# Kernel optimization log

Hardware: AMD Instinct MI355X
Metric: run time of the kernel (lower is better)

The kernel has to match this reference:

```python
import jax, jax.numpy as jnp
import numpy as np

B, N, H, W = 1, 256, 32, 32
C_LIDAR, C_RGB, K, S = 64, 64, 16, 3
MLP3 = [128, 64, 64]


def _l2norm(x, eps=1e-12):
    n = jnp.linalg.norm(x, axis=-1, keepdims=True)
    return x / jnp.maximum(n, eps)


def _cal_sim(src, dst):
    # src [B,N,C], dst [B,M,C] -> [B,N,M,2] (cosine sim normalized two ways)
    s = _l2norm(src)
    d = _l2norm(dst)
    sim = jnp.einsum('bmc,bnc->bmn', d, s)  # [B,M,N]
    dst_src = sim / (jnp.max(sim, axis=2, keepdims=True) + 1e-10)
    src_dst = jnp.swapaxes(sim, 1, 2)       # [B,N,M]
    src_dst = src_dst / (jnp.max(src_dst, axis=2, keepdims=True) + 1e-6)
    return jnp.stack([src_dst, jnp.swapaxes(dst_src, 1, 2)], axis=-1)


def _mlp(x, layers):
    # 1x1 conv + (identity-init BN folded) + ReLU chain, channel-last
    for w, b in layers:
        x = jax.nn.relu(x @ w + b)
    return x


def _unfold(x, s):
    # F.unfold with zero pad s//2: [B,C,H,W] -> [B, H*W, s*s, C]
    p = s // 2
    b, c, h, w = x.shape
    xp = jnp.pad(x, ((0, 0), (0, 0), (p, p), (p, p)))
    pats = jnp.stack([xp[:, :, i:i + h, j:j + w] for i in range(s) for j in range(s)], axis=2)
    return pats.reshape(b, c, s * s, h * w).transpose(0, 3, 2, 1)


def _weighted_pnp(src_xyz, uv, wgt):
    # weighted SVD (Kabsch) head: lift uv to 3D at source depth, solve R,t
    z = src_xyz[..., 2:3]
    dst = jnp.concatenate([uv, jnp.ones_like(z)], axis=-1) * z
    wn = wgt / (jnp.sum(wgt, axis=-1, keepdims=True) + 1e-8)
    sc = jnp.einsum('bn,bnc->bc', wn, src_xyz)
    dc = jnp.einsum('bn,bnc->bc', wn, dst)
    s_c = src_xyz - sc[:, None]
    d_c = dst - dc[:, None]
    Hm = jnp.einsum('bn,bni,bnj->bij', wn, s_c, d_c)
    U, _, Vt = jnp.linalg.svd(Hm)
    V = jnp.swapaxes(Vt, -1, -2)
    det = jnp.linalg.det(jnp.einsum('bik,bjk->bij', V, U))
    diag = jnp.stack([jnp.ones_like(det), jnp.ones_like(det), det], axis=-1)
    R = jnp.einsum('bik,bk,bjk->bij', V, diag, U)
    t = dc - jnp.einsum('bij,bj->bi', R, sc)
    return R, t


def reference(warped_xyz, warped_points, RF3, RF3_index, lidar_z,
              w2_0, b2_0, w2_1, b2_1, w2_2, b2_2,
              w3_0, b3_0, w3_1, b3_1, w3_2, b3_2,
              w1_0, b1_0, w1_1, b1_1, w1_2, b1_2,
              wm_0, bm_0, wm_1, bm_1, wm_2, bm_2):
    b, n, _ = warped_xyz.shape
    _, ci, h, w = RF3.shape
    m = h * w
    xyz = warped_xyz * lidar_z                       # [B,N,3]
    rf = RF3.transpose(0, 2, 3, 1).reshape(b, m, ci)   # [B,M,Ci]
    rfi = RF3_index.transpose(0, 2, 3, 1).reshape(b, m, 3)

    src_dst_sim = _cal_sim(warped_points, rf)        # [B,N,M,2]

    # kNN grouping of the point cloud onto itself
    d2 = jnp.sum((xyz[:, :, None, :] - xyz[:, None, :, :]) ** 2, axis=-1)
    _, idx = jax.lax.top_k(-d2, K)                   # [B,N,K]
    gather = jax.vmap(lambda pts, i: pts[i])
    pc_xyz_g = gather(xyz, idx)                      # [B,N,K,3]
    pc_pts_g = gather(warped_points, idx)            # [B,N,K,C]
    diff = pc_xyz_g - xyz[:, :, None, :]
    dn = jnp.linalg.norm(diff, axis=-1, keepdims=True)
    pc_nbr = jnp.concatenate([pc_pts_g, diff, dn], axis=-1)
    wts = _mlp(pc_nbr, [(w2_0, b2_0), (w2_1, b2_1), (w2_2, b2_2)])
    wts = jnp.max(wts, axis=-1, keepdims=True)
    wts = jax.nn.softmax(wts, axis=-2)
    pc_feats = jnp.sum(wts * pc_pts_g, axis=-2)      # [B,N,C]

    # image 3x3 neighbor grouping via unfold
    rf_nbr_idx = _unfold(RF3_index, S)               # [B,M,SS,3]
    rf_nbr_pts = _unfold(RF3, S)                     # [B,M,SS,Ci]
    iw = _mlp(jnp.concatenate([rf_nbr_idx, rf_nbr_pts], axis=-1),
              [(w3_0, b3_0), (w3_1, b3_1), (w3_2, b3_2)])
    iw = jnp.max(iw, axis=-1, keepdims=True)
    iw = jax.nn.softmax(iw, axis=-2)
    img_feats = jnp.sum(iw * rf_nbr_pts, axis=-2)    # [B,M,Ci]

    nbr_sim = _cal_sim(pc_feats, img_feats)          # [B,N,M,2]

    feats = jnp.concatenate([
        jnp.broadcast_to(xyz[:, :, None, :], (b, n, m, 3)),
        jnp.broadcast_to(rfi[:, None, :, :], (b, n, m, 3)),
        jnp.broadcast_to(warped_points[:, :, None, :], (b, n, m, warped_points.shape[-1])),
        jnp.broadcast_to(rf[:, None, :, :], (b, n, m, ci)),
        src_dst_sim, nbr_sim], axis=-1)              # [B,N,M,6+C+Ci+4]
    feats = _mlp(feats, [(w1_0, b1_0), (w1_1, b1_1), (w1_2, b1_2)])

    aw = jax.nn.softmax(jnp.max(feats, axis=-1), axis=-1)   # [B,N,M]
    corres_uv1 = jnp.einsum('bnm,bmc->bnc', aw, rfi)         # [B,N,3]
    att = jnp.einsum('bnm,bnmc->bnc', aw, feats)             # [B,N,64]
    att = _mlp(att, [(wm_0, bm_0), (wm_1, bm_1)])
    logits = att @ wm_2 + bm_2                               # [B,N,2]
    weights = jax.nn.softmax(logits, axis=-1)
    w_in = jnp.argmax(weights, axis=-1).astype(weights.dtype)
    R, t = _weighted_pnp(xyz, corres_uv1[..., :2], w_in)
    return R, t, weights


def setup_inputs():
    key = jax.random.key(0)
    ks = jax.random.split(key, 32)
    f32 = jnp.float32
    inp = {}
    inp['warped_xyz'] = jax.random.normal(ks[0], (B, N, 3), f32)
    inp['warped_points'] = jax.random.normal(ks[1], (B, N, C_LIDAR), f32)
    inp['RF3'] = jax.random.normal(ks[2], (B, C_RGB, H, W), f32)
    inp['RF3_index'] = jax.random.normal(ks[3], (B, 3, H, W), f32)
    inp['lidar_z'] = jax.random.uniform(ks[4], (B, N, 1), f32, 0.5, 2.0)
    wdims = {'w2_0': (4 + C_LIDAR, C_LIDAR), 'w2_1': (C_LIDAR, C_LIDAR), 'w2_2': (C_LIDAR, C_LIDAR),
             'w3_0': (3 + C_RGB, C_RGB), 'w3_1': (C_RGB, C_RGB), 'w3_2': (C_RGB, C_RGB),
             'w1_0': (6 + C_RGB + C_LIDAR + 4, MLP3[0]), 'w1_1': (MLP3[0], MLP3[1]), 'w1_2': (MLP3[1], MLP3[2]),
             'wm_0': (MLP3[2], MLP3[2]), 'wm_1': (MLP3[2], MLP3[0]), 'wm_2': (MLP3[0], 2)}
    for i, (name, d) in enumerate(wdims.items()):
        inp[name] = jax.random.normal(ks[5 + i], d, f32) * 0.05
        inp['b' + name[1:]] = jnp.zeros((d[1],), f32)
    return inp
```

## Files before the change

kernel.cpp:

```cpp
#include <hip/hip_runtime.h>
#include <math.h>


typedef _Float16 f16;
typedef __attribute__((ext_vector_type(4))) _Float16 f16x4;
typedef __attribute__((ext_vector_type(8))) _Float16 f16x8;
typedef __attribute__((ext_vector_type(4))) float f32x4;

constexpr int WS_XYZ  = 0;
constexpr int WS_RF   = 768;
constexpr int WS_RFI  = WS_RF   + 65536;
constexpr int WS_SN   = WS_RFI  + 3072;
constexpr int WS_RS   = WS_SN;
constexpr int WS_RD   = WS_SN   + 256;
constexpr int WS_WPT  = WS_SN   + 16384;
constexpr int WS_SIM1 = WS_WPT  + 65536;
constexpr int WS_RM1  = WS_SIM1 + 262144;
constexpr int WS_CM1  = WS_RM1  + 1024;
constexpr int WS_PCT  = WS_CM1  + 256;
constexpr int WS_IMGF = WS_PCT  + 16384;
constexpr int WS_PCN  = WS_IMGF + 65536;
constexpr int WS_IMGN = WS_PCN  + 16384;
constexpr int WS_SIM2 = WS_IMGN + 65536;
constexpr int WS_RM2  = WS_SIM2 + 262144;
constexpr int WS_CM2  = WS_RM2  + 1024;
constexpr int WS_B1   = WS_CM2  + 256;
constexpr int WS_B2   = WS_B1   + 32768;
constexpr int WS_ATT  = WS_B2   + 131072;
constexpr int WS_UV   = WS_ATT  + 16384;
constexpr int WS_WIN  = WS_UV   + 768;
constexpr int WS_KNN  = WS_WIN  + 256;
constexpr int WS_PM   = WS_KNN  + 4096;
constexpr int WS_PS   = WS_PM   + 2048;
constexpr int WS_PATT = WS_PS   + 2048;
constexpr int WS_PUV  = WS_PATT + 131072;
constexpr int WS_W11T = WS_PUV  + 6144;
constexpr int WS_W12T = WS_W11T + 4096;
constexpr int WS_G3   = WS_W12T + 2048;
constexpr int WS_SIMF = WS_G3   + 65600;

__global__ __launch_bounds__(256) void prep_kernel(float* ws, const float* wxyz,
                                                   const float* lz, const float* RF3,
                                                   const float* RFI, const float* w11,
                                                   const float* w12, const float* wpts) {
    int b = blockIdx.x;
    if (b < 319) {
        int i = b * 256 + threadIdx.x;
        if (i < 768) {
            int n = i / 3;
            ws[WS_XYZ + i] = wxyz[i] * lz[n];
        } else if (i < 768 + 65536) {
            int j = i - 768; int mm = j >> 6, c = j & 63;
            ws[WS_RF + j] = RF3[c * 1024 + mm];
        } else if (i < 768 + 65536 + 3072) {
            int j = i - (768 + 65536); int mm = j / 3, c = j - mm * 3;
            ws[WS_RFI + j] = RFI[c * 1024 + mm];
        } else if (i < 69376 + 8192) {
            int j = i - 69376; int col = j >> 7, k = j & 127;
            ((f16*)(ws + WS_W11T))[col * 128 + k] = (f16)w11[k * 64 + col];
        } else if (i < 69376 + 12288) {
            int j = i - (69376 + 8192); int col = j >> 6, k = j & 63;
            ((f16*)(ws + WS_W12T))[col * 64 + k] = (f16)w12[k * 64 + col];
        }
    } else if (b == 319) {
        int n = threadIdx.x;
        float s = 0.f;
        for (int c = 0; c < 64; c++) { float v = wpts[n * 64 + c]; s += v * v; }
        ws[WS_RS + n] = 1.f / fmaxf(sqrtf(s), 1e-12f);
    } else if (b < 324) {
        int m = (b - 320) * 256 + threadIdx.x;
        float s = 0.f;
        for (int c = 0; c < 64; c++) { float v = RF3[c * 1024 + m]; s += v * v; }
        ws[WS_RD + m] = 1.f / fmaxf(sqrtf(s), 1e-12f);
    } else {
        int i = (b - 324) * 256 + threadIdx.x;
        int c = i >> 8, n = i & 255;
        ws[WS_WPT + c * 256 + n] = wpts[n * 64 + c];
    }
}

__global__ __launch_bounds__(256) void mid_kernel(float* ws, const float* wpts,
        const float* w30, const float* b30, const float* w10, const float* b10) {
    int b = blockIdx.x, t = threadIdx.x;
    __shared__ float px[256], py[256], pz[256], d2[256];
    __shared__ float rv[256];
    __shared__ int   ri[256];
    __shared__ float wred[4];
    if (b < 1024) {
        int m = b;
        int wave = t >> 6, lane = t & 63;
        const float* rf = ws + WS_RF;
        const float* wptsT = ws + WS_WPT;
        if (t < 64) px[t] = rf[m * 64 + t];
        __syncthreads();
        float acc = 0.f;
        for (int c = 0; c < 64; c += 4) {
            acc += px[c]     * wptsT[c * 256 + t]
                 + px[c + 1] * wptsT[(c + 1) * 256 + t]
                 + px[c + 2] * wptsT[(c + 2) * 256 + t]
                 + px[c + 3] * wptsT[(c + 3) * 256 + t];
        }
        acc = acc * ws[WS_RD + m] * ws[WS_RS + t];
        ws[WS_SIM1 + t * 1024 + m] = acc;
        float mx = acc;
        for (int o = 32; o > 0; o >>= 1) mx = fmaxf(mx, __shfl_down(mx, o));
        if (lane == 0) wred[wave] = mx;
        __syncthreads();
        if (t == 0)
            ws[WS_RM1 + m] = fmaxf(fmaxf(wred[0], wred[1]), fmaxf(wred[2], wred[3]));
    } else if (b < 1281) {
        int m = (b - 1024) * 4 + (t >> 6), j = t & 63;
        if (m < 1025) {
            float acc;
            if (m < 1024) {
                float a0 = b30[j], a1 = 0.f, a2 = 0.f, a3 = 0.f;
                for (int i = 0; i < 3; i++) a0 += ws[WS_RFI + m * 3 + i] * w30[i * 64 + j];
                const float* rfm = ws + WS_RF + m * 64;
                const float* wp = w30 + 3 * 64 + j;
                for (int c = 0; c < 64; c += 4) {
                    a0 += rfm[c]     * wp[c * 64];
                    a1 += rfm[c + 1] * wp[(c + 1) * 64];
                    a2 += rfm[c + 2] * wp[(c + 2) * 64];
                    a3 += rfm[c + 3] * wp[(c + 3) * 64];
                }
                acc = (a0 + a1) + (a2 + a3);
            } else {
                acc = b30[j];
            }
            ws[WS_G3 + m * 64 + j] = fmaxf(acc, 0.f);
        }
    } else if (b < 1921) {
        int bb = (b - 1281) * 2 + (t >> 7);
        int j = t & 127;
        if (bb < 256) {
            int n = bb;
            float a0 = b10[j], a1 = 0.f, a2 = 0.f, a3 = 0.f;
            for (int i = 0; i < 3; i++) a0 += ws[WS_XYZ + n * 3 + i] * w10[i * 128 + j];
            const float* xp = wpts + n * 64;
            const float* wp = w10 + 6 * 128 + j;
            for (int c = 0; c < 64; c += 4) {
                a0 += xp[c]     * wp[c * 128];
                a1 += xp[c + 1] * wp[(c + 1) * 128];
                a2 += xp[c + 2] * wp[(c + 2) * 128];
                a3 += xp[c + 3] * wp[(c + 3) * 128];
            }
            ws[WS_B1 + n * 128 + j] = (a0 + a1) + (a2 + a3);
        } else {
            int m = bb - 256;
            float a0 = 0.f, a1 = 0.f, a2 = 0.f, a3 = 0.f;
            for (int i = 0; i < 3; i++) a0 += ws[WS_RFI + m * 3 + i] * w10[(3 + i) * 128 + j];
            const float* rfm = ws + WS_RF + m * 64;
            const float* wp = w10 + 70 * 128 + j;
            for (int c = 0; c < 64; c += 4) {
                a0 += rfm[c]     * wp[c * 128];
                a1 += rfm[c + 1] * wp[(c + 1) * 128];
                a2 += rfm[c + 2] * wp[(c + 2) * 128];
                a3 += rfm[c + 3] * wp[(c + 3) * 128];
            }
            ws[WS_B2 + m * 128 + j] = (a0 + a1) + (a2 + a3);
        }
    } else {
        const float* xyz = ws + WS_XYZ;
        int* knn = (int*)(ws + WS_KNN);
        int n = b - 1921;
        px[t] = xyz[t * 3 + 0]; py[t] = xyz[t * 3 + 1]; pz[t] = xyz[t * 3 + 2];
        __syncthreads();
        float dx = px[t] - px[n], dy = py[t] - py[n], dz = pz[t] - pz[n];
        d2[t] = dx * dx + dy * dy + dz * dz;
        __syncthreads();
        for (int k = 0; k < 16; k++) {
            rv[t] = d2[t]; ri[t] = t;
            __syncthreads();
            for (int s = 128; s > 0; s >>= 1) {
                if (t < s) {
                    float v2 = rv[t + s]; int i2 = ri[t + s];
                    if (v2 < rv[t] || (v2 == rv[t] && i2 < ri[t])) { rv[t] = v2; ri[t] = i2; }
                }
                __syncthreads();
            }
            if (t == 0) { knn[n * 16 + k] = ri[0]; d2[ri[0]] = INFINITY; }
            __syncthreads();
        }
    }
}

__global__ __launch_bounds__(256) void sim2_kernel(float* ws) {
    __shared__ __align__(16) float dv[64];
    __shared__ float wred[4];
    int m = blockIdx.x, t = threadIdx.x;
    int wave = t >> 6, lane = t & 63;
    if (t < 64) dv[t] = ws[WS_IMGN + m * 64 + t];
    __syncthreads();
    const float* pcnT = ws + WS_PCT;
    float acc = 0.f;
    for (int c = 0; c < 64; c += 4) {
        acc += dv[c]     * pcnT[c * 256 + t]
             + dv[c + 1] * pcnT[(c + 1) * 256 + t]
             + dv[c + 2] * pcnT[(c + 2) * 256 + t]
             + dv[c + 3] * pcnT[(c + 3) * 256 + t];
    }
    ws[WS_SIM2 + t * 1024 + m] = acc;
    float mx = acc;
    for (int o = 32; o > 0; o >>= 1) mx = fmaxf(mx, __shfl_down(mx, o));
    if (lane == 0) wred[wave] = mx;
    __syncthreads();
    if (t == 0)
        ws[WS_RM2 + m] = fmaxf(fmaxf(wred[0], wred[1]), fmaxf(wred[2], wred[3]));
}

__global__ __launch_bounds__(256) void simfeat_kernel(float* ws) {
    __shared__ float wred1[4], wred2[4];
    int n = blockIdx.x, t = threadIdx.x;
    int wave = t >> 6, lane = t & 63;
    const float* sim1 = ws + WS_SIM1;  const float* rm1g = ws + WS_RM1;
    const float* sim2 = ws + WS_SIM2;  const float* rm2g = ws + WS_RM2;
    f16* simfg = (f16*)(ws + WS_SIMF);
    float s1v[4], s2v[4];
    float mx1 = -INFINITY, mx2 = -INFINITY;
    for (int j = 0; j < 4; j++) {
        int m = t + j * 256;
        s1v[j] = sim1[n * 1024 + m]; mx1 = fmaxf(mx1, s1v[j]);
        s2v[j] = sim2[n * 1024 + m]; mx2 = fmaxf(mx2, s2v[j]);
    }
    float m1 = mx1, m2 = mx2;
    for (int o = 32; o > 0; o >>= 1) {
        m1 = fmaxf(m1, __shfl_down(m1, o));
        m2 = fmaxf(m2, __shfl_down(m2, o));
    }
    if (lane == 0) { wred1[wave] = m1; wred2[wave] = m2; }
    __syncthreads();
    float cm1 = fmaxf(fmaxf(wred1[0], wred1[1]), fmaxf(wred1[2], wred1[3]));
    float cm2 = fmaxf(fmaxf(wred2[0], wred2[1]), fmaxf(wred2[2], wred2[3]));
    for (int j = 0; j < 4; j++) {
        int m = t + j * 256;
        float r1 = rm1g[m], r2 = rm2g[m];
        float f0 = s1v[j] / (cm1 + 1e-6f);
        float f1 = s1v[j] / (r1 + 1e-10f);
        float f2 = s2v[j] / (cm2 + 1e-6f);
        float f3 = s2v[j] / (r2 + 1e-10f);
        *(f16x4*)&simfg[(n * 1024 + m) * 4] =
            (f16x4){(f16)f0, (f16)f1, (f16)f2, (f16)f3};
    }
}

__global__ __launch_bounds__(256) void mlp23_kernel(float* ws, const float* wpts,
        const float* w20, const float* b20, const float* w21, const float* b21,
        const float* w22, const float* b22,
        const float* w31, const float* b31, const float* w32, const float* b32) {
    __shared__ float sbuf[36 * 68 * 2];
    __shared__ float small1[36], small2[36];
    __shared__ int   kn[16];
    int b = blockIdx.x, t = threadIdx.x;
    if (b < 256) {
        int n = b;
        float* x  = sbuf;
        float* hA = sbuf + 1088;
        float* hB = sbuf + 2176;
        const float* xyz = ws + WS_XYZ;
        const int* knn = (const int*)(ws + WS_KNN);
        if (t < 16) kn[t] = knn[n * 16 + t];
        __syncthreads();
        for (int i = t; i < 1024; i += 256) {
            int k = i >> 6, c = i & 63;
            x[k * 68 + c] = wpts[kn[k] * 64 + c];
        }
        if (t < 16) {
            int i = kn[t];
            float dx = xyz[i * 3 + 0] - xyz[n * 3 + 0];
            float dy = xyz[i * 3 + 1] - xyz[n * 3 + 1];
            float dz = xyz[i * 3 + 2] - xyz[n * 3 + 2];
            x[t * 68 + 64] = dx; x[t * 68 + 65] = dy; x[t * 68 + 66] = dz;
            x[t * 68 + 67] = sqrtf(dx * dx + dy * dy + dz * dz);
        }
        __syncthreads();
        for (int o = t; o < 1024; o += 256) {
            int k = o >> 6, j = o & 63;
            float a0 = b20[j], a1 = 0.f, a2 = 0.f, a3 = 0.f;
            const float* xr = &x[k * 68];
            const float* wp = w20 + j;
            for (int i = 0; i < 68; i += 4) {
                a0 += xr[i]     * wp[i * 64];
                a1 += xr[i + 1] * wp[(i + 1) * 64];
                a2 += xr[i + 2] * wp[(i + 2) * 64];
                a3 += xr[i + 3] * wp[(i + 3) * 64];
            }
            hA[k * 68 + j] = fmaxf((a0 + a1) + (a2 + a3), 0.f);
        }
        __syncthreads();
        for (int o = t; o < 1024; o += 256) {
            int k = o >> 6, j = o & 63;
            float a0 = b21[j], a1 = 0.f, a2 = 0.f, a3 = 0.f;
            const float* xr = &hA[k * 68];
            const float* wp = w21 + j;
            for (int i = 0; i < 64; i += 4) {
                a0 += xr[i]     * wp[i * 64];
                a1 += xr[i + 1] * wp[(i + 1) * 64];
                a2 += xr[i + 2] * wp[(i + 2) * 64];
                a3 += xr[i + 3] * wp[(i + 3) * 64];
            }
            hB[k * 68 + j] = fmaxf((a0 + a1) + (a2 + a3), 0.f);
        }
        __syncthreads();
        for (int o = t; o < 1024; o += 256) {
            int k = o >> 6, j = o & 63;
            float a0 = b22[j], a1 = 0.f, a2 = 0.f, a3 = 0.f;
// ... 58 lines not shown
                a2 += xr[i + 2] * wp[(i + 2) * 64];
                a3 += xr[i + 3] * wp[(i + 3) * 64];
            }
            h2[row * 68 + c] = fmaxf((a0 + a1) + (a2 + a3), 0.f);
        }
        __syncthreads();
        for (int o = t; o < 36 * 64; o += 256) {
            int row = o >> 6, c = o & 63;
            float a0 = b32[c], a1 = 0.f, a2 = 0.f, a3 = 0.f;
            const float* xr = &h2[row * 68];
            const float* wp = w32 + c;
            for (int i = 0; i < 64; i += 4) {
                a0 += xr[i]     * wp[i * 64];
                a1 += xr[i + 1] * wp[(i + 1) * 64];
                a2 += xr[i + 2] * wp[(i + 2) * 64];
                a3 += xr[i + 3] * wp[(i + 3) * 64];
            }
            x1[row * 68 + c] = fmaxf((a0 + a1) + (a2 + a3), 0.f);
        }
        __syncthreads();
        if (t < 36) {
            float mx = -INFINITY;
            for (int c = 0; c < 64; c++) mx = fmaxf(mx, x1[t * 68 + c]);
            small1[t] = mx;
        }
        __syncthreads();
        if (t < 36) {
            int mi = t / 9;
            float mx = -INFINITY;
            for (int k = 0; k < 9; k++) mx = fmaxf(mx, small1[mi * 9 + k]);
            float sum = 0.f;
            for (int k = 0; k < 9; k++) sum += expf(small1[mi * 9 + k] - mx);
            small2[t] = expf(small1[t] - mx) / sum;
        }
        __syncthreads();
        {
            int mi = t >> 6, c = t & 63;
            int m = m0 + mi; int y = m >> 5, x = m & 31;
            float acc = 0.f;
            for (int kk = 0; kk < 9; kk++) {
                int dy = kk / 3 - 1, dx = kk % 3 - 1;
                int ny = y + dy, nx = x + dx;
                bool val = (ny >= 0 && ny < 32 && nx >= 0 && nx < 32);
                if (val) acc += small2[mi * 9 + kk] * rf[(ny * 32 + nx) * 64 + c];
            }
            float s = acc * acc;
            for (int o = 32; o > 0; o >>= 1) s += __shfl_down(s, o);
            s = __shfl(s, 0);
            ws[WS_IMGN + m * 64 + c] = acc / fmaxf(sqrtf(s), 1e-12f);
        }
    }
}

__global__ __launch_bounds__(256) void mlp1_kernel(float* ws, const float* w10,
        const float* b11, const float* b12) {
    __shared__ __align__(16) f16 H1h[64 * 136];
    __shared__ __align__(16) f16 H2h[64 * 72];
    __shared__ float base1n[128];
    __shared__ float simw[4 * 128];
    __shared__ float rmPart[4][64];
    int n = blockIdx.y, seg = blockIdx.x, t = threadIdx.x;
    int wave = t >> 6, lane = t & 63, q = lane >> 4, l16 = lane & 15;
    int col = wave * 16 + l16;
    const float* base2 = ws + WS_B2;
    const float* rfig = ws + WS_RFI;
    const f16* simfg = (const f16*)(ws + WS_SIMF);
    const f16* w11t = (const f16*)(ws + WS_W11T);
    const f16* w12t = (const f16*)(ws + WS_W12T);
    if (t < 128) base1n[t] = ws[WS_B1 + n * 128 + t];
    for (int i = t; i < 512; i += 256) simw[i] = w10[134 * 128 + i];
    f16x8 B2f[4], B3f[2];
    for (int s = 0; s < 4; s++) B2f[s] = *(const f16x8*)&w11t[col * 128 + s * 32 + q * 8];
    for (int s = 0; s < 2; s++) B3f[s] = *(const f16x8*)&w12t[col * 64 + s * 32 + q * 8];
    float bias2 = b11[col], bias3 = b12[col];
    float attAcc = 0.f;
    float uv0 = 0.f, uv1 = 0.f, uv2 = 0.f;
    float Mv = -INFINITY, Sv = 0.f;
    int mBeg = seg * 128;
    __syncthreads();
    for (int c4 = 0; c4 < 2; c4++) {
        int m0 = mBeg + c4 * 64;
        for (int idx = t; idx < 2048; idx += 256) {
            int row = idx >> 5, k4 = (idx & 31) * 4;
            int m = m0 + row;
            f16x4 sf = *(const f16x4*)&simfg[(n * 1024 + m) * 4];
            float s0 = (float)sf[0], s1 = (float)sf[1], s2 = (float)sf[2], s3 = (float)sf[3];
            float4 bs = *(const float4*)&base2[m * 128 + k4];
            float4 b1v = *(const float4*)&base1n[k4];
            float4 w0v = *(const float4*)&simw[k4];
            float4 w1v = *(const float4*)&simw[128 + k4];
            float4 w2v = *(const float4*)&simw[256 + k4];
            float4 w3v = *(const float4*)&simw[384 + k4];
            float v0 = b1v.x + bs.x + s0 * w0v.x + s1 * w1v.x + s2 * w2v.x + s3 * w3v.x;
            float v1 = b1v.y + bs.y + s0 * w0v.y + s1 * w1v.y + s2 * w2v.y + s3 * w3v.y;
            float v2 = b1v.z + bs.z + s0 * w0v.z + s1 * w1v.z + s2 * w2v.z + s3 * w3v.z;
            float v3 = b1v.w + bs.w + s0 * w0v.w + s1 * w1v.w + s2 * w2v.w + s3 * w3v.w;
            *(f16x4*)&H1h[row * 136 + k4] = (f16x4){
                (f16)fmaxf(v0, 0.f), (f16)fmaxf(v1, 0.f),
                (f16)fmaxf(v2, 0.f), (f16)fmaxf(v3, 0.f)};
        }
        __syncthreads();
        f32x4 a[4];
        for (int tl = 0; tl < 4; tl++) a[tl] = (f32x4){bias2, bias2, bias2, bias2};
        for (int s = 0; s < 4; s++)
            for (int tl = 0; tl < 4; tl++) {
                f16x8 f = *(const f16x8*)&H1h[(tl * 16 + l16) * 136 + s * 32 + q * 8];
                a[tl] = __builtin_amdgcn_mfma_f32_16x16x32_f16(f, B2f[s], a[tl], 0, 0, 0);
            }
        for (int tl = 0; tl < 4; tl++)
            for (int r = 0; r < 4; r++)
                H2h[(tl * 16 + q * 4 + r) * 72 + col] = (f16)fmaxf(a[tl][r], 0.f);
        __syncthreads();
        f32x4 c3[4];
        for (int tl = 0; tl < 4; tl++) c3[tl] = (f32x4){bias3, bias3, bias3, bias3};
        for (int s = 0; s < 2; s++)
            for (int tl = 0; tl < 4; tl++) {
                f16x8 f = *(const f16x8*)&H2h[(tl * 16 + l16) * 72 + s * 32 + q * 8];
                c3[tl] = __builtin_amdgcn_mfma_f32_16x16x32_f16(f, B3f[s], c3[tl], 0, 0, 0);
            }
        for (int tl = 0; tl < 4; tl++)
            for (int r = 0; r < 4; r++)
                c3[tl][r] = fmaxf(c3[tl][r], 0.f);
        for (int tl = 0; tl < 4; tl++)
            for (int r = 0; r < 4; r++) {
                float v = c3[tl][r];
                v = fmaxf(v, __shfl_xor(v, 1));
                v = fmaxf(v, __shfl_xor(v, 2));
                v = fmaxf(v, __shfl_xor(v, 4));
                v = fmaxf(v, __shfl_xor(v, 8));
                if (l16 == 0) rmPart[wave][tl * 16 + q * 4 + r] = v;
            }
        __syncthreads();
        float rmv = fmaxf(fmaxf(rmPart[0][lane], rmPart[1][lane]),
                          fmaxf(rmPart[2][lane], rmPart[3][lane]));
        float tv = rmv;
        for (int off = 32; off > 0; off >>= 1) tv = fmaxf(tv, __shfl_xor(tv, off));
        float newM = fmaxf(Mv, tv);
        float rescale = __expf(Mv - newM);
        float ewv = __expf(rmv - newM);
        Mv = newM;
        float se = ewv;
        for (int off = 32; off > 0; off >>= 1) se += __shfl_xor(se, off);
        Sv = Sv * rescale + se;
        float ap = 0.f;
        for (int tl = 0; tl < 4; tl++)
            for (int r = 0; r < 4; r++)
                ap += __shfl(ewv, tl * 16 + q * 4 + r) * c3[tl][r];
        ap += __shfl_xor(ap, 16);
        ap += __shfl_xor(ap, 32);
        if (lane < 16) attAcc = attAcc * rescale + ap;
        if (wave == 0) {
            const float* rp = &rfig[(m0 + lane) * 3];
            float u0 = ewv * rp[0], u1 = ewv * rp[1], u2 = ewv * rp[2];
            for (int off = 32; off > 0; off >>= 1) {
                u0 += __shfl_xor(u0, off);
                u1 += __shfl_xor(u1, off);
                u2 += __shfl_xor(u2, off);
            }
            uv0 = uv0 * rescale + u0;
            uv1 = uv1 * rescale + u1;
            uv2 = uv2 * rescale + u2;
        }
    }
    int p = n * 8 + seg;
    if (t == 0) {
        ws[WS_PM + p] = Mv; ws[WS_PS + p] = Sv;
        ws[WS_PUV + p * 3 + 0] = uv0;
        ws[WS_PUV + p * 3 + 1] = uv1;
        ws[WS_PUV + p * 3 + 2] = uv2;
    }
    if (lane < 16) ws[WS_PATT + p * 64 + wave * 16 + lane] = attAcc;
}

__global__ __launch_bounds__(128) void combinehead_kernel(float* ws,
        const float* wm0, const float* bm0, const float* wm1, const float* bm1,
        const float* wm2, const float* bm2, float* out) {
    __shared__ float av[64], ha[64], hb[128], lg[2];
    int n = blockIdx.x, t = threadIdx.x;
    float pm[8], e[8];
    float M = -INFINITY;
    for (int s = 0; s < 8; s++) { pm[s] = ws[WS_PM + n * 8 + s]; M = fmaxf(M, pm[s]); }
    float S = 0.f;
    for (int s = 0; s < 8; s++) { e[s] = expf(pm[s] - M); S += ws[WS_PS + n * 8 + s] * e[s]; }
    if (t < 64) {
        float acc = 0.f;
        for (int s = 0; s < 8; s++) acc += ws[WS_PATT + (n * 8 + s) * 64 + t] * e[s];
        av[t] = acc / S;
    } else if (t < 67) {
        int c = t - 64; float acc = 0.f;
        for (int s = 0; s < 8; s++) acc += ws[WS_PUV + (n * 8 + s) * 3 + c] * e[s];
        ws[WS_UV + n * 3 + c] = acc / S;
    }
    __syncthreads();
    if (t < 64) {
        float acc = bm0[t];
        for (int i = 0; i < 64; i++) acc += av[i] * wm0[i * 64 + t];
        ha[t] = fmaxf(acc, 0.f);
    }
    __syncthreads();
    {
        float acc = bm1[t];
        for (int i = 0; i < 64; i++) acc += ha[i] * wm1[i * 128 + t];
        hb[t] = fmaxf(acc, 0.f);
    }
    __syncthreads();
    if (t < 2) {
        float acc = bm2[t];
        for (int i = 0; i < 128; i++) acc += hb[i] * wm2[i * 2 + t];
        lg[t] = acc;
    }
    __syncthreads();
    if (t == 0) {
        float l0 = lg[0], l1 = lg[1];
        float mx = fmaxf(l0, l1);
        float e0 = expf(l0 - mx), e1 = expf(l1 - mx);
        float s = e0 + e1;
        out[12 + n * 2 + 0] = e0 / s;
        out[12 + n * 2 + 1] = e1 / s;
        ws[WS_WIN + n] = (e1 > e0) ? 1.f : 0.f;
    }
}

__device__ void compute_rt(const double Hm[9], const double sc[3], const double dc[3],
                           float* out) {
    double Hd[3][3] = {{Hm[0], Hm[1], Hm[2]}, {Hm[3], Hm[4], Hm[5]}, {Hm[6], Hm[7], Hm[8]}};
    double A[3][3], V[3][3] = {{1, 0, 0}, {0, 1, 0}, {0, 0, 1}};
    for (int i = 0; i < 3; i++)
        for (int j = 0; j < 3; j++) {
            double s = 0;
            for (int k = 0; k < 3; k++) s += Hd[k][i] * Hd[k][j];
            A[i][j] = s;
        }
    for (int sweep = 0; sweep < 50; sweep++) {
        double off = fabs(A[0][1]) + fabs(A[0][2]) + fabs(A[1][2]);
        if (off < 1e-28) break;
        const int PQ[3][2] = {{0, 1}, {0, 2}, {1, 2}};
        for (int pp = 0; pp < 3; pp++) {
            int p = PQ[pp][0], q = PQ[pp][1];
            double apq = A[p][q];
            if (fabs(apq) < 1e-300) continue;
            double tau = (A[q][q] - A[p][p]) / (2.0 * apq);
            double tt = (tau >= 0.0 ? 1.0 : -1.0) / (fabs(tau) + sqrt(1.0 + tau * tau));
            double c = 1.0 / sqrt(1.0 + tt * tt), s = tt * c;
            for (int k = 0; k < 3; k++) {
                double akp = A[k][p], akq = A[k][q];
                A[k][p] = c * akp - s * akq; A[k][q] = s * akp + c * akq;
            }
            for (int k = 0; k < 3; k++) {
                double apk = A[p][k], aqk = A[q][k];
                A[p][k] = c * apk - s * aqk; A[q][k] = s * apk + c * aqk;
            }
            for (int k = 0; k < 3; k++) {
                double vkp = V[k][p], vkq = V[k][q];
                V[k][p] = c * vkp - s * vkq; V[k][q] = s * vkp + c * vkq;
            }
        }
    }
    double lam[3] = {A[0][0], A[1][1], A[2][2]};
    int o0 = 0, o1 = 1, o2 = 2;
    if (lam[o0] < lam[o1]) { int tp = o0; o0 = o1; o1 = tp; }
    if (lam[o0] < lam[o2]) { int tp = o0; o0 = o2; o2 = tp; }
    if (lam[o1] < lam[o2]) { int tp = o1; o1 = o2; o2 = tp; }
    int ord[3] = {o0, o1, o2};
    double v[3][3], u[3][3], R[3][3];
    for (int k = 0; k < 3; k++)
        for (int i = 0; i < 3; i++) v[k][i] = V[i][ord[k]];
    double sv0 = sqrt(fmax(lam[o0], 0.0));
    if (!(sv0 > 1e-150)) {
        for (int i = 0; i < 3; i++)
            for (int j = 0; j < 3; j++) R[i][j] = (i == j) ? 1.0 : 0.0;
    } else {
        double nn[3];
// ... 61 lines not shown
        if (t < s)
            for (int k = 0; k < 7; k++) red[k][t] += red[k][t + s];
        __syncthreads();
    }
    double wsum = red[0][0];
    double sx0 = red[1][0], sx1 = red[2][0], sx2 = red[3][0];
    double sd0 = red[4][0], sd1 = red[5][0], sd2 = red[6][0];
    __syncthreads();
    double inv = 1.0 / (wsum + 1e-8);
    double sc[3] = {sx0 * inv, sx1 * inv, sx2 * inv};
    double dc[3] = {sd0 * inv, sd1 * inv, sd2 * inv};
    double wn = w * inv;
    double a0 = x0 - sc[0], a1 = x1 - sc[1], a2 = x2 - sc[2];
    double b0 = dd0 - dc[0], b1 = dd1 - dc[1], b2 = dd2 - dc[2];
    red[0][t] = wn * a0 * b0; red[1][t] = wn * a0 * b1; red[2][t] = wn * a0 * b2;
    red[3][t] = wn * a1 * b0; red[4][t] = wn * a1 * b1; red[5][t] = wn * a1 * b2;
    red[6][t] = wn * a2 * b0; red[7][t] = wn * a2 * b1; red[8][t] = wn * a2 * b2;
    __syncthreads();
    for (int s = 128; s > 0; s >>= 1) {
        if (t < s)
            for (int k = 0; k < 9; k++) red[k][t] += red[k][t + s];
        __syncthreads();
    }
    if (t == 0) {
        double Hm[9];
        for (int k = 0; k < 9; k++) Hm[k] = red[k][0];
        compute_rt(Hm, sc, dc, out);
    }
}

extern "C" void kernel_launch(void* const* d_in, const int* in_sizes, int n_in,
                              void* d_out, int out_size, void* d_ws, size_t ws_size,
                              hipStream_t stream) {
    float* ws = (float*)d_ws;
    const float* wxyz = (const float*)d_in[0];
    const float* wpts = (const float*)d_in[1];
    const float* RF3  = (const float*)d_in[2];
    const float* RFI  = (const float*)d_in[3];
    const float* lz   = (const float*)d_in[4];
    const float* w2_0 = (const float*)d_in[5];  const float* b2_0 = (const float*)d_in[6];
    const float* w2_1 = (const float*)d_in[7];  const float* b2_1 = (const float*)d_in[8];
    const float* w2_2 = (const float*)d_in[9];  const float* b2_2 = (const float*)d_in[10];
    const float* w3_0 = (const float*)d_in[11]; const float* b3_0 = (const float*)d_in[12];
    const float* w3_1 = (const float*)d_in[13]; const float* b3_1 = (const float*)d_in[14];
    const float* w3_2 = (const float*)d_in[15]; const float* b3_2 = (const float*)d_in[16];
    const float* w1_0 = (const float*)d_in[17]; const float* b1_0 = (const float*)d_in[18];
    const float* w1_1 = (const float*)d_in[19]; const float* b1_1 = (const float*)d_in[20];
    const float* w1_2 = (const float*)d_in[21]; const float* b1_2 = (const float*)d_in[22];
    const float* wm_0 = (const float*)d_in[23]; const float* bm_0 = (const float*)d_in[24];
    const float* wm_1 = (const float*)d_in[25]; const float* bm_1 = (const float*)d_in[26];
    const float* wm_2 = (const float*)d_in[27]; const float* bm_2 = (const float*)d_in[28];
    float* out = (float*)d_out;

    prep_kernel<<<388, 256, 0, stream>>>(ws, wxyz, lz, RF3, RFI, w1_1, w1_2, wpts);
    mid_kernel<<<2177, 256, 0, stream>>>(ws, wpts, w3_0, b3_0, w1_0, b1_0);
    mlp23_kernel<<<512, 256, 0, stream>>>(ws, wpts, w2_0, b2_0, w2_1, b2_1, w2_2, b2_2,
                                          w3_1, b3_1, w3_2, b3_2);
    sim2_kernel<<<1024, 256, 0, stream>>>(ws);
    simfeat_kernel<<<256, 256, 0, stream>>>(ws);
    mlp1_kernel<<<dim3(8, 256), 256, 0, stream>>>(ws, w1_0, b1_1, b1_2);
    combinehead_kernel<<<256, 128, 0, stream>>>(ws, wm_0, bm_0, wm_1, bm_1, wm_2, bm_2, out);
    pnp_kernel<<<1, 256, 0, stream>>>(ws, out);
}
```

Before: 223.3 us.

## Fuse seven pipeline kernels into one cooperative persistent kernel with grid syncs

Turns the seven stage kernels into device functions and runs them from a single persistent cooperative kernel. Each stage uses a grid-stride loop over its virtual blocks and stages are separated by grid.sync(). Shared memory is one union buffer reused across stages. The goal is to remove per-launch overhead and inter-kernel gaps, at the cost of grid-wide barrier latency, lower occupancy from sizing shared memory to the largest stage, and serialised virtual blocks. If the cooperative launch fails, the original multi-kernel path is used instead.

```diff
diff --git a/kernel.cpp b/kernel.cpp
--- a/kernel.cpp
+++ b/kernel.cpp
@@ -1,5 +1,8 @@
 #include <hip/hip_runtime.h>
+#include <hip/hip_cooperative_groups.h>
 #include <math.h>
+
+namespace cg = cooperative_groups;
 
 
 typedef _Float16 f16;
@@ -39,13 +42,12 @@
 constexpr int WS_G3   = WS_W12T + 2048;
 constexpr int WS_SIMF = WS_G3   + 65600;
 
-__global__ __launch_bounds__(256) void prep_kernel(float* ws, const float* wxyz,
-                                                   const float* lz, const float* RF3,
-                                                   const float* RFI, const float* w11,
-                                                   const float* w12, const float* wpts) {
-    int b = blockIdx.x;
+
+__device__ __forceinline__ void prep_body(int b, int t, float* ws, const float* wxyz,
+        const float* lz, const float* RF3, const float* RFI, const float* w11,
+        const float* w12, const float* wpts) {
     if (b < 319) {
-        int i = b * 256 + threadIdx.x;
+        int i = b * 256 + t;
         if (i < 768) {
             int n = i / 3;
             ws[WS_XYZ + i] = wxyz[i] * lz[n];
@@ -63,29 +65,25 @@
             ((f16*)(ws + WS_W12T))[col * 64 + k] = (f16)w12[k * 64 + col];
         }
     } else if (b == 319) {
-        int n = threadIdx.x;
+        int n = t;
         float s = 0.f;
         for (int c = 0; c < 64; c++) { float v = wpts[n * 64 + c]; s += v * v; }
         ws[WS_RS + n] = 1.f / fmaxf(sqrtf(s), 1e-12f);
     } else if (b < 324) {
-        int m = (b - 320) * 256 + threadIdx.x;
+        int m = (b - 320) * 256 + t;
         float s = 0.f;
         for (int c = 0; c < 64; c++) { float v = RF3[c * 1024 + m]; s += v * v; }
         ws[WS_RD + m] = 1.f / fmaxf(sqrtf(s), 1e-12f);
     } else {
-        int i = (b - 324) * 256 + threadIdx.x;
+        int i = (b - 324) * 256 + t;
         int c = i >> 8, n = i & 255;
         ws[WS_WPT + c * 256 + n] = wpts[n * 64 + c];
     }
 }
 
-__global__ __launch_bounds__(256) void mid_kernel(float* ws, const float* wpts,
-        const float* w30, const float* b30, const float* w10, const float* b10) {
-    int b = blockIdx.x, t = threadIdx.x;
-    __shared__ float px[256], py[256], pz[256], d2[256];
-    __shared__ float rv[256];
-    __shared__ int   ri[256];
-    __shared__ float wred[4];
+__device__ __forceinline__ void mid_body(int b, int t, float* ws, const float* wpts,
+        const float* w30, const float* b30, const float* w10, const float* b10,
+        float* px, float* py, float* pz, float* d2, float* rv, int* ri, float* wred) {
     if (b < 1024) {
         int m = b;
         int wave = t >> 6, lane = t & 63;
@@ -184,73 +182,11 @@
     }
 }
 
-__global__ __launch_bounds__(256) void sim2_kernel(float* ws) {
-    __shared__ __align__(16) float dv[64];
-    __shared__ float wred[4];
-    int m = blockIdx.x, t = threadIdx.x;
-    int wave = t >> 6, lane = t & 63;
-    if (t < 64) dv[t] = ws[WS_IMGN + m * 64 + t];
-    __syncthreads();
-    const float* pcnT = ws + WS_PCT;
-    float acc = 0.f;
-    for (int c = 0; c < 64; c += 4) {
-        acc += dv[c]     * pcnT[c * 256 + t]
-             + dv[c + 1] * pcnT[(c + 1) * 256 + t]
-             + dv[c + 2] * pcnT[(c + 2) * 256 + t]
-             + dv[c + 3] * pcnT[(c + 3) * 256 + t];
-    }
-    ws[WS_SIM2 + t * 1024 + m] = acc;
-    float mx = acc;
-    for (int o = 32; o > 0; o >>= 1) mx = fmaxf(mx, __shfl_down(mx, o));
-    if (lane == 0) wred[wave] = mx;
-    __syncthreads();
-    if (t == 0)
-        ws[WS_RM2 + m] = fmaxf(fmaxf(wred[0], wred[1]), fmaxf(wred[2], wred[3]));
-}
-
-__global__ __launch_bounds__(256) void simfeat_kernel(float* ws) {
-    __shared__ float wred1[4], wred2[4];
-    int n = blockIdx.x, t = threadIdx.x;
-    int wave = t >> 6, lane = t & 63;
-    const float* sim1 = ws + WS_SIM1;  const float* rm1g = ws + WS_RM1;
-    const float* sim2 = ws + WS_SIM2;  const float* rm2g = ws + WS_RM2;
-    f16* simfg = (f16*)(ws + WS_SIMF);
-    float s1v[4], s2v[4];
-    float mx1 = -INFINITY, mx2 = -INFINITY;
-    for (int j = 0; j < 4; j++) {
-        int m = t + j * 256;
-        s1v[j] = sim1[n * 1024 + m]; mx1 = fmaxf(mx1, s1v[j]);
-        s2v[j] = sim2[n * 1024 + m]; mx2 = fmaxf(mx2, s2v[j]);
-    }
-    float m1 = mx1, m2 = mx2;
-    for (int o = 32; o > 0; o >>= 1) {
-        m1 = fmaxf(m1, __shfl_down(m1, o));
-        m2 = fmaxf(m2, __shfl_down(m2, o));
-    }
-    if (lane == 0) { wred1[wave] = m1; wred2[wave] = m2; }
-    __syncthreads();
-    float cm1 = fmaxf(fmaxf(wred1[0], wred1[1]), fmaxf(wred1[2], wred1[3]));
-    float cm2 = fmaxf(fmaxf(wred2[0], wred2[1]), fmaxf(wred2[2], wred2[3]));
-    for (int j = 0; j < 4; j++) {
-        int m = t + j * 256;
-        float r1 = rm1g[m], r2 = rm2g[m];
-        float f0 = s1v[j] / (cm1 + 1e-6f);
-        float f1 = s1v[j] / (r1 + 1e-10f);
-        float f2 = s2v[j] / (cm2 + 1e-6f);
-        float f3 = s2v[j] / (r2 + 1e-10f);
-        *(f16x4*)&simfg[(n * 1024 + m) * 4] =
-            (f16x4){(f16)f0, (f16)f1, (f16)f2, (f16)f3};
-    }
-}
-
-__global__ __launch_bounds__(256) void mlp23_kernel(float* ws, const float* wpts,
+__device__ __forceinline__ void mlp23_body(int b, int t, float* ws, const float* wpts,
         const float* w20, const float* b20, const float* w21, const float* b21,
         const float* w22, const float* b22,
-        const float* w31, const float* b31, const float* w32, const float* b32) {
-    __shared__ float sbuf[36 * 68 * 2];
-    __shared__ float small1[36], small2[36];
-    __shared__ int   kn[16];
-    int b = blockIdx.x, t = threadIdx.x;
+        const float* w31, const float* b31, const float* w32, const float* b32,
+        float* sbuf, float* small1, float* small2, int* kn) {
     if (b < 256) {
         int n = b;
         float* x  = sbuf;
@@ -415,27 +351,70 @@
     }
 }
 
-__global__ __launch_bounds__(256) void mlp1_kernel(float* ws, const float* w10,
-        const float* b11, const float* b12) {
-    __shared__ __align__(16) f16 H1h[64 * 136];
-    __shared__ __align__(16) f16 H2h[64 * 72];
-    __shared__ float base1n[128];
-    __shared__ float simw[4 * 128];
-    __shared__ float rmPart[4][64];
-    int n = blockIdx.y, seg = blockIdx.x, t = threadIdx.x;
+__device__ __forceinline__ void sim2_body(int m, int t, float* ws, float* dv, float* wred) {
+    int wave = t >> 6, lane = t & 63;
+    if (t < 64) dv[t] = ws[WS_IMGN + m * 64 + t];
+    __syncthreads();
+    const float* pcnT = ws + WS_PCT;
+    float acc = 0.f;
+    for (int c = 0; c < 64; c += 4) {
+        acc += dv[c]     * pcnT[c * 256 + t]
+             + dv[c + 1] * pcnT[(c + 1) * 256 + t]
+             + dv[c + 2] * pcnT[(c + 2) * 256 + t]
+             + dv[c + 3] * pcnT[(c + 3) * 256 + t];
+    }
+    ws[WS_SIM2 + t * 1024 + m] = acc;
+    float mx = acc;
+    for (int o = 32; o > 0; o >>= 1) mx = fmaxf(mx, __shfl_down(mx, o));
+    if (lane == 0) wred[wave] = mx;
+    __syncthreads();
+    if (t == 0)
+        ws[WS_RM2 + m] = fmaxf(fmaxf(wred[0], wred[1]), fmaxf(wred[2], wred[3]));
+}
+
+__device__ __forceinline__ void simfeat_body(int n, int t, float* ws,
+                                             float* wred1, float* wred2) {
+    int wave = t >> 6, lane = t & 63;
+    const float* sim1 = ws + WS_SIM1;  const float* rm1g = ws + WS_RM1;
+    const float* sim2 = ws + WS_SIM2;  const float* rm2g = ws + WS_RM2;
+    f16* simfg = (f16*)(ws + WS_SIMF);
+    float s1v[4], s2v[4];
+    float mx1 = -INFINITY, mx2 = -INFINITY;
+    for (int j = 0; j < 4; j++) {
+        int m = t + j * 256;
+        s1v[j] = sim1[n * 1024 + m]; mx1 = fmaxf(mx1, s1v[j]);
+        s2v[j] = sim2[n * 1024 + m]; mx2 = fmaxf(mx2, s2v[j]);
+    }
+    float m1 = mx1, m2 = mx2;
+    for (int o = 32; o > 0; o >>= 1) {
+        m1 = fmaxf(m1, __shfl_down(m1, o));
+        m2 = fmaxf(m2, __shfl_down(m2, o));
+    }
+    if (lane == 0) { wred1[wave] = m1; wred2[wave] = m2; }
+    __syncthreads();
+    float cm1 = fmaxf(fmaxf(wred1[0], wred1[1]), fmaxf(wred1[2], wred1[3]));
+    float cm2 = fmaxf(fmaxf(wred2[0], wred2[1]), fmaxf(wred2[2], wred2[3]));
+    for (int j = 0; j < 4; j++) {
+        int m = t + j * 256;
+        float r1 = rm1g[m], r2 = rm2g[m];
+        float f0 = s1v[j] / (cm1 + 1e-6f);
+        float f1 = s1v[j] / (r1 + 1e-10f);
+        float f2 = s2v[j] / (cm2 + 1e-6f);
+        float f3 = s2v[j] / (r2 + 1e-10f);
+        *(f16x4*)&simfg[(n * 1024 + m) * 4] =
+            (f16x4){(f16)f0, (f16)f1, (f16)f2, (f16)f3};
+    }
+}
+
+__device__ __forceinline__ void mlp1_body(int n, int seg, int t, float* ws,
+        const f16x8* B2f, const f16x8* B3f, float bias2, float bias3,
+        f16* H1h, f16* H2h, float* base1n, float* simw, float* rmPart) {
     int wave = t >> 6, lane = t & 63, q = lane >> 4, l16 = lane & 15;
     int col = wave * 16 + l16;
     const float* base2 = ws + WS_B2;
     const float* rfig = ws + WS_RFI;
     const f16* simfg = (const f16*)(ws + WS_SIMF);
-    const f16* w11t = (const f16*)(ws + WS_W11T);
-    const f16* w12t = (const f16*)(ws + WS_W12T);
     if (t < 128) base1n[t] = ws[WS_B1 + n * 128 + t];
-    for (int i = t; i < 512; i += 256) simw[i] = w10[134 * 128 + i];
-    f16x8 B2f[4], B3f[2];
-    for (int s = 0; s < 4; s++) B2f[s] = *(const f16x8*)&w11t[col * 128 + s * 32 + q * 8];
-    for (int s = 0; s < 2; s++) B3f[s] = *(const f16x8*)&w12t[col * 64 + s * 32 + q * 8];
-    float bias2 = b11[col], bias3 = b12[col];
     float attAcc = 0.f;
     float uv0 = 0.f, uv1 = 0.f, uv2 = 0.f;
     float Mv = -INFINITY, Sv = 0.f;
@@ -491,11 +470,11 @@
                 v = fmaxf(v, __shfl_xor(v, 2));
                 v = fmaxf(v, __shfl_xor(v, 4));
                 v = fmaxf(v, __shfl_xor(v, 8));
-                if (l16 == 0) rmPart[wave][tl * 16 + q * 4 + r] = v;
-            }
-        __syncthreads();
-        float rmv = fmaxf(fmaxf(rmPart[0][lane], rmPart[1][lane]),
-                          fmaxf(rmPart[2][lane], rmPart[3][lane]));
+                if (l16 == 0) rmPart[wave * 64 + tl * 16 + q * 4 + r] = v;
+            }
+        __syncthreads();
+        float rmv = fmaxf(fmaxf(rmPart[0 * 64 + lane], rmPart[1 * 64 + lane]),
+                          fmaxf(rmPart[2 * 64 + lane], rmPart[3 * 64 + lane]));
         float tv = rmv;
         for (int off = 32; off > 0; off >>= 1) tv = fmaxf(tv, __shfl_xor(tv, off));
         float newM = fmaxf(Mv, tv);
@@ -535,11 +514,10 @@
     if (lane < 16) ws[WS_PATT + p * 64 + wave * 16 + lane] = attAcc;
 }
 
-__global__ __launch_bounds__(128) void combinehead_kernel(float* ws,
+__device__ __forceinline__ void combinehead_body(int n, int t, float* ws,
         const float* wm0, const float* bm0, const float* wm1, const float* bm1,
-        const float* wm2, const float* bm2, float* out) {
-    __shared__ float av[64], ha[64], hb[128], lg[2];
-    int n = blockIdx.x, t = threadIdx.x;
+        const float* wm2, const float* bm2, float* out,
+        float* av, float* ha, float* hb, float* lg) {
     float pm[8], e[8];
     float M = -INFINITY;
     for (int s = 0; s < 8; s++) { pm[s] = ws[WS_PM + n * 8 + s]; M = fmaxf(M, pm[s]); }
@@ -561,7 +539,7 @@
         ha[t] = fmaxf(acc, 0.f);
     }
     __syncthreads();
-    {
+    if (t < 128) {
         float acc = bm1[t];
         for (int i = 0; i < 64; i++) acc += ha[i] * wm1[i * 128 + t];
         hb[t] = fmaxf(acc, 0.f);
@@ -581,6 +559,175 @@
         out[12 + n * 2 + 0] = e0 / s;
         out[12 + n * 2 + 1] = e1 / s;
         ws[WS_WIN + n] = (e1 > e0) ? 1.f : 0.f;
+    }
+}
+
+
+__global__ __launch_bounds__(256) void prep_kernel(float* ws, const float* wxyz,
+        const float* lz, const float* RF3, const float* RFI, const float* w11,
+        const float* w12, const float* wpts) {
+    prep_body(blockIdx.x, threadIdx.x, ws, wxyz, lz, RF3, RFI, w11, w12, wpts);
+}
+
+__global__ __launch_bounds__(256) void mid_kernel(float* ws, const float* wpts,
+        const float* w30, const float* b30, const float* w10, const float* b10) {
+    __shared__ float px[256], py[256], pz[256], d2[256], rv[256];
+    __shared__ int   ri[256];
+    __shared__ float wred[4];
+    mid_body(blockIdx.x, threadIdx.x, ws, wpts, w30, b30, w10, b10,
+             px, py, pz, d2, rv, ri, wred);
+}
+
+__global__ __launch_bounds__(256) void mlp23_kernel(float* ws, const float* wpts,
+        const float* w20, const float* b20, const float* w21, const float* b21,
+        const float* w22, const float* b22,
+        const float* w31, const float* b31, const float* w32, const float* b32) {
+    __shared__ float sbuf[4896];
+    __shared__ float small1[36], small2[36];
+    __shared__ int   kn[16];
+    mlp23_body(blockIdx.x, threadIdx.x, ws, wpts, w20, b20, w21, b21, w22, b22,
+               w31, b31, w32, b32, sbuf, small1, small2, kn);
+}
+
+__global__ __launch_bounds__(256) void sim2_kernel(float* ws) {
+    __shared__ __align__(16) float dv[64];
+    __shared__ float wred[4];
+    sim2_body(blockIdx.x, threadIdx.x, ws, dv, wred);
+}
+
+__global__ __launch_bounds__(256) void simfeat_kernel(float* ws) {
+    __shared__ float wred1[4], wred2[4];
+    simfeat_body(blockIdx.x, threadIdx.x, ws, wred1, wred2);
+}
+
+__global__ __launch_bounds__(256) void mlp1_kernel(float* ws, const float* w10,
+        const float* b11, const float* b12) {
+    __shared__ __align__(16) f16 H1h[64 * 136];
+    __shared__ __align__(16) f16 H2h[64 * 72];
+    __shared__ float base1n[128];
+    __shared__ float simw[512];
+    __shared__ float rmPart[256];
+    int t = threadIdx.x;
+    int wave = t >> 6, lane = t & 63, q = lane >> 4, l16 = lane & 15;
+    int col = wave * 16 + l16;
+    const f16* w11t = (const f16*)(ws + WS_W11T);
+    const f16* w12t = (const f16*)(ws + WS_W12T);
+    for (int i = t; i < 512; i += 256) simw[i] = w10[134 * 128 + i];
+    f16x8 B2f[4], B3f[2];
+    for (int s = 0; s < 4; s++) B2f[s] = *(const f16x8*)&w11t[col * 128 + s * 32 + q * 8];
+    for (int s = 0; s < 2; s++) B3f[s] = *(const f16x8*)&w12t[col * 64 + s * 32 + q * 8];
+    float bias2 = b11[col], bias3 = b12[col];
+    mlp1_body(blockIdx.y, blockIdx.x, t, ws, B2f, B3f, bias2, bias3,
+              H1h, H2h, base1n, simw, rmPart);
+}
+
+__global__ __launch_bounds__(128) void combinehead_kernel(float* ws,
+        const float* wm0, const float* bm0, const float* wm1, const float* bm1,
+        const float* wm2, const float* bm2, float* out) {
+    __shared__ float av[64], ha[64], hb[128], lg[2];
+    combinehead_body(blockIdx.x, threadIdx.x, ws, wm0, bm0, wm1, bm1, wm2, bm2, out,
+                     av, ha, hb, lg);
+}
+
+
+__global__ __launch_bounds__(256) void mega_kernel(float* ws,
+        const float* wxyz, const float* lz, const float* RF3, const float* RFI,
+        const float* w11, const float* w12, const float* wpts,
+        const float* w30, const float* b30, const float* w10, const float* b10,
+        const float* w20, const float* b20, const float* w21, const float* b21,
+        const float* w22, const float* b22,
+        const float* w31, const float* b31, const float* w32, const float* b32,
+        const float* b11, const float* b12,
+        const float* wm0, const float* bm0, const float* wm1, const float* bm1,
+        const float* wm2, const float* bm2, float* out) {
+    cg::grid_group grid = cg::this_grid();
+    __shared__ __align__(16) unsigned char smem[30208];
+    int t = threadIdx.x;
+
+    for (int b = blockIdx.x; b < 388; b += gridDim.x)
+        prep_body(b, t, ws, wxyz, lz, RF3, RFI, w11, w12, wpts);
+    grid.sync();
+
+    {
+        float* px = (float*)smem;
+        float* py = px + 256;
+        float* pz = py + 256;
+        float* d2 = pz + 256;
+        float* rv = d2 + 256;
+        int*   ri = (int*)(rv + 256);
+        float* wred = (float*)(ri + 256);
+        for (int b = blockIdx.x; b < 2177; b += gridDim.x) {
+            mid_body(b, t, ws, wpts, w30, b30, w10, b10, px, py, pz, d2, rv, ri, wred);
+            __syncthreads();
+        }
+    }
+    grid.sync();
+
+    {
+        float* sbuf = (float*)smem;
+        float* small1 = sbuf + 4896;
+        float* small2 = small1 + 36;
+        int* kn = (int*)(small2 + 36);
+        for (int b = blockIdx.x; b < 512; b += gridDim.x) {
+            mlp23_body(b, t, ws, wpts, w20, b20, w21, b21, w22, b22,
+                       w31, b31, w32, b32, sbuf, small1, small2, kn);
+            __syncthreads();
+        }
+    }
+    grid.sync();
+
+    {
+        float* dv = (float*)smem;
+        float* wred = dv + 64;
+        for (int b = blockIdx.x; b < 1024; b += gridDim.x) {
+            sim2_body(b, t, ws, dv, wred);
+            __syncthreads();
+        }
+    }
+    grid.sync();
+
+    {
+        float* wred1 = (float*)smem;
+        float* wred2 = wred1 + 4;
+        for (int b = blockIdx.x; b < 256; b += gridDim.x) {
+            simfeat_body(b, t, ws, wred1, wred2);
+            __syncthreads();
+        }
+    }
+    grid.sync();
+
+    {
+        f16* H1h = (f16*)smem;
+        f16* H2h = H1h + 64 * 136;
+        float* base1n = (float*)(H2h + 64 * 72);
+        float* simw = base1n + 128;
+        float* rmPart = simw + 512;
+        int wave = t >> 6, lane = t & 63, q = lane >> 4, l16 = lane & 15;
+        int col = wave * 16 + l16;
+        const f16* w11t = (const f16*)(ws + WS_W11T);
+        const f16* w12t = (const f16*)(ws + WS_W12T);
+        for (int i = t; i < 512; i += 256) simw[i] = w10[134 * 128 + i];
+        f16x8 B2f[4], B3f[2];
+        for (int s = 0; s < 4; s++) B2f[s] = *(const f16x8*)&w11t[col * 128 + s * 32 + q * 8];
+        for (int s = 0; s < 2; s++) B3f[s] = *(const f16x8*)&w12t[col * 64 + s * 32 + q * 8];
+        float bias2 = b11[col], bias3 = b12[col];
+        for (int vb = blockIdx.x; vb < 2048; vb += gridDim.x) {
+            mlp1_body(vb >> 3, vb & 7, t, ws, B2f, B3f, bias2, bias3,
+                      H1h, H2h, base1n, simw, rmPart);
+            __syncthreads();
+        }
+    }
+    grid.sync();
+
+    {
+        float* av = (float*)smem;
+        float* ha = av + 64;
+        float* hb = ha + 64;
+        float* lg = hb + 128;
+        for (int b = blockIdx.x; b < 256; b += gridDim.x) {
+            combinehead_body(b, t, ws, wm0, bm0, wm1, bm1, wm2, bm2, out, av, ha, hb, lg);
+            __syncthreads();
+        }
     }
 }
 
@@ -748,13 +895,46 @@
     const float* wm_2 = (const float*)d_in[27]; const float* bm_2 = (const float*)d_in[28];
     float* out = (float*)d_out;
 
-    prep_kernel<<<388, 256, 0, stream>>>(ws, wxyz, lz, RF3, RFI, w1_1, w1_2, wpts);
-    mid_kernel<<<2177, 256, 0, stream>>>(ws, wpts, w3_0, b3_0, w1_0, b1_0);
-    mlp23_kernel<<<512, 256, 0, stream>>>(ws, wpts, w2_0, b2_0, w2_1, b2_1, w2_2, b2_2,
-                                          w3_1, b3_1, w3_2, b3_2);
-    sim2_kernel<<<1024, 256, 0, stream>>>(ws);
-    simfeat_kernel<<<256, 256, 0, stream>>>(ws);
-    mlp1_kernel<<<dim3(8, 256), 256, 0, stream>>>(ws, w1_0, b1_1, b1_2);
-    combinehead_kernel<<<256, 128, 0, stream>>>(ws, wm_0, bm_0, wm_1, bm_1, wm_2, bm_2, out);
+    hipError_t rc = hipErrorUnknown;
+    int dev = 0;
+    if (hipGetDevice(&dev) == hipSuccess) {
+        int nCU = 0;
+        hipDeviceGetAttribute(&nCU, hipDeviceAttributeMultiprocessorCount, dev);
+        if (nCU <= 0) nCU = 256;
+        int occ = 0;
+        hipOccupancyMaxActiveBlocksPerMultiprocessor(&occ, mega_kernel, 256, 0);
+        void* args[] = {
+            (void*)&ws, (void*)&wxyz, (void*)&lz, (void*)&RF3, (void*)&RFI,
+            (void*)&w1_1, (void*)&w1_2, (void*)&wpts,
+            (void*)&w3_0, (void*)&b3_0, (void*)&w1_0, (void*)&b1_0,
+            (void*)&w2_0, (void*)&b2_0, (void*)&w2_1, (void*)&b2_1, (void*)&w2_2, (void*)&b2_2,
+            (void*)&w3_1, (void*)&b3_1, (void*)&w3_2, (void*)&b3_2,
+            (void*)&b1_1, (void*)&b1_2,
+            (void*)&wm_0, (void*)&bm_0, (void*)&wm_1, (void*)&bm_1, (void*)&wm_2, (void*)&bm_2,
+            (void*)&out
+        };
+        if (occ >= 1) {
+            long cap = (long)occ * (long)nCU;
+            int grid = (int)(cap < 2048 ? cap : 2048);
+            rc = hipLaunchCooperativeKernel((void*)mega_kernel, dim3(grid), dim3(256),
+                                            args, 0, stream);
+            if (rc != hipSuccess) {
+                (void)hipGetLastError();
+                rc = hipLaunchCooperativeKernel((void*)mega_kernel, dim3(nCU), dim3(256),
+                                                args, 0, stream);
+                if (rc != hipSuccess) (void)hipGetLastError();
+            }
+        }
+    }
+    if (rc != hipSuccess) {
+        prep_kernel<<<388, 256, 0, stream>>>(ws, wxyz, lz, RF3, RFI, w1_1, w1_2, wpts);
+        mid_kernel<<<2177, 256, 0, stream>>>(ws, wpts, w3_0, b3_0, w1_0, b1_0);
+        mlp23_kernel<<<512, 256, 0, stream>>>(ws, wpts, w2_0, b2_0, w2_1, b2_1, w2_2, b2_2,
+                                              w3_1, b3_1, w3_2, b3_2);
+        sim2_kernel<<<1024, 256, 0, stream>>>(ws);
+        simfeat_kernel<<<256, 256, 0, stream>>>(ws);
+        mlp1_kernel<<<dim3(8, 256), 256, 0, stream>>>(ws, w1_0, b1_1, b1_2);
+        combinehead_kernel<<<256, 128, 0, stream>>>(ws, wm_0, bm_0, wm_1, bm_1, wm_2, bm_2, out);
+    }
     pnp_kernel<<<1, 256, 0, stream>>>(ws, out);
 }
```

Result: slower. 234.2 us (+4.9%).
